# Performance work log

Hardware: AMD Instinct MI355X
Metric: run time of the kernel (lower is better)

Reference implementation:

```python
import jax, jax.numpy as jnp
import numpy as np
import math

DIM = 2048
N_HEADS = 32
N_KV_HEADS = 8
HEAD_DIM = DIM // N_HEADS  # 64
N_REP = N_HEADS // N_KV_HEADS  # 4
BATCH = 1
SEQ = 2048


def rope_cos_sin(seq_len, head_dim, dtype=jnp.float32):
    inv_freq = 1.0 / (10000.0 ** (jnp.arange(0, head_dim, 2, dtype=jnp.float32) / head_dim))
    t = jnp.arange(seq_len, dtype=jnp.float32)
    freqs = jnp.outer(t, inv_freq)            # [S, D/2]
    emb = jnp.concatenate([freqs, freqs], -1)  # [S, D]
    return jnp.cos(emb).astype(dtype), jnp.sin(emb).astype(dtype)


def rotate_half(x):
    x1 = x[..., ::2]
    x2 = x[..., 1::2]
    return jnp.concatenate([-x2, x1], axis=-1)


def setup_inputs() -> dict:
    key = jax.random.key(0)
    ks = jax.random.split(key, 5)
    scale = 1.0 / math.sqrt(DIM)
    x = jax.random.normal(ks[0], (BATCH, SEQ, DIM), jnp.float32)
    wq = jax.random.normal(ks[1], (DIM, N_HEADS * HEAD_DIM), jnp.float32) * scale
    wk = jax.random.normal(ks[2], (DIM, N_KV_HEADS * HEAD_DIM), jnp.float32) * scale
    wv = jax.random.normal(ks[3], (DIM, N_KV_HEADS * HEAD_DIM), jnp.float32) * scale
    wo = jax.random.normal(ks[4], (N_HEADS * HEAD_DIM, DIM), jnp.float32) * scale
    mask = jnp.tril(jnp.ones((SEQ, SEQ), jnp.int32))[None, None]  # [1,1,S,S]
    return {"x": x, "mask": mask, "wq": wq, "wk": wk, "wv": wv, "wo": wo}


def reference(x, mask, wq, wk, wv, wo):
    B, S, _ = x.shape
    q = (x @ wq).reshape(B, S, N_HEADS, HEAD_DIM).transpose(0, 2, 1, 3)     # [B,H,S,D]
    k = (x @ wk).reshape(B, S, N_KV_HEADS, HEAD_DIM).transpose(0, 2, 1, 3)  # [B,Hkv,S,D]
    v = (x @ wv).reshape(B, S, N_KV_HEADS, HEAD_DIM).transpose(0, 2, 1, 3)
    cos, sin = rope_cos_sin(S, HEAD_DIM)  # [S,D]
    q = q * cos + rotate_half(q) * sin
    k = k * cos + rotate_half(k) * sin
    if N_REP > 1:
        k = jnp.repeat(k, N_REP, axis=1)
        v = jnp.repeat(v, N_REP, axis=1)
    scores = jnp.einsum("bhqd,bhkd->bhqk", q, k) / math.sqrt(HEAD_DIM)
    scores = jnp.where(mask == 0, -jnp.inf, scores)
    attn = jax.nn.softmax(scores, axis=-1)
    out = jnp.einsum("bhqk,bhkd->bhqd", attn, v)  # [B,H,S,D]
    out = out.transpose(0, 2, 1, 3).reshape(B, S, N_HEADS * HEAD_DIM)
    return out @ wo
```

## Files before the change

### kernel.cpp

```cpp
#include <hip/hip_runtime.h>
#include <hip/hip_bf16.h>

#define DIM 2048
#define SEQ 2048
#define NH 32
#define HD 64
#define NKV 8
#define QKV_LD 3072

typedef __attribute__((ext_vector_type(8))) short bf16x8;
typedef __attribute__((ext_vector_type(4))) float f32x4;
typedef unsigned short ushort_t;

__device__ inline unsigned short f2bf(float f) {
    union { float f; unsigned int u; } v; v.f = f;
    unsigned int r = v.u + 0x7fffu + ((v.u >> 16) & 1u);
    return (unsigned short)(r >> 16);
}
__device__ inline float bf2f(ushort_t u) {
    union { unsigned int u; float f; } v; v.u = ((unsigned int)u) << 16; return v.f;
}

__device__ inline void async_cp16(const void* g, void* l) {
    __builtin_amdgcn_global_load_lds(
        (const __attribute__((address_space(1))) unsigned int*)g,
        (__attribute__((address_space(3))) unsigned int*)l, 16, 0, 0);
}
__device__ inline void lgkm_fence() {
    __asm__ volatile("s_waitcnt lgkmcnt(0)" ::: "memory");
}

__global__ __launch_bounds__(256) void convert_kernel(
    const float* __restrict__ X, ushort_t* __restrict__ Xb)
{
    int i = (blockIdx.x * 256 + threadIdx.x) * 4;
    float4 v = *(const float4*)(X + i);
    ushort_t o[4] = { f2bf(v.x), f2bf(v.y), f2bf(v.z), f2bf(v.w) };
    *(uint2*)(Xb + i) = *(uint2*)o;
}

__global__ __launch_bounds__(256) void transpose_kernel(
    const float* __restrict__ W, ushort_t* __restrict__ WT, int N)
{
    __shared__ __align__(16) ushort_t tile[64][72];
    const int n0 = blockIdx.x * 64, k0 = blockIdx.y * 64;
    const int t = threadIdx.x;
    {
        const int tk = t >> 4;
        const int tn = (t & 15) * 4;
        #pragma unroll
        for (int i = 0; i < 4; i++) {
            const int k = tk + i * 16;
            float4 v = *(const float4*)(W + (size_t)(k0 + k) * N + n0 + tn);
            tile[tn + 0][k] = f2bf(v.x);
            tile[tn + 1][k] = f2bf(v.y);
            tile[tn + 2][k] = f2bf(v.z);
            tile[tn + 3][k] = f2bf(v.w);
        }
    }
    __syncthreads();
    {
        const int tn = t >> 2;
        const int tk = (t & 3) * 16;
        uint4 a = *(const uint4*)&tile[tn][tk];
        uint4 b = *(const uint4*)&tile[tn][tk + 8];
        ushort_t* dst = WT + (size_t)(n0 + tn) * DIM + k0 + tk;
        *(uint4*)dst = a;
        *(uint4*)(dst + 8) = b;
    }
}

template<int OUT_F32>
__global__ __launch_bounds__(256) void gemm_kernel(
    const ushort_t* __restrict__ A, const ushort_t* __restrict__ BT,
    void* __restrict__ Cout, int K, int lda, int ldo)
{
    __shared__ __align__(16) ushort_t sA[128 * 32];
    __shared__ __align__(16) ushort_t sB[128 * 32];
    const int tn = blockIdx.x * 128, tm = blockIdx.y * 128;
    const int t = threadIdx.x, wave = t >> 6, lane = t & 63;
    const int m16 = lane & 15, quad = lane >> 4;
    const int wr = (wave >> 1) * 64, wc = (wave & 1) * 64;
    const int srow = lane >> 2;
    const int sce = (lane & 3) * 8;

    f32x4 acc[4][4] = {};

    for (int k0 = 0; k0 < K; k0 += 32) {
        __syncthreads();
        #pragma unroll
        for (int p = 0; p < 2; p++) {
            const int j = wave * 2 + p;
            const int row = j * 16 + srow;
            async_cp16(A  + (size_t)(tm + row) * lda + k0 + sce, &sA[j * 512]);
            async_cp16(BT + (size_t)(tn + row) * K   + k0 + sce, &sB[j * 512]);
        }
        __syncthreads();
        bf16x8 af[4], bf[4];
        #pragma unroll
        for (int mt = 0; mt < 4; mt++)
            af[mt] = *(const bf16x8*)&sA[(wr + mt * 16 + m16) * 32 + quad * 8];
        #pragma unroll
        for (int nt = 0; nt < 4; nt++)
            bf[nt] = *(const bf16x8*)&sB[(wc + nt * 16 + m16) * 32 + quad * 8];
        #pragma unroll
        for (int mt = 0; mt < 4; mt++)
            #pragma unroll
            for (int nt = 0; nt < 4; nt++)
                acc[mt][nt] = __builtin_amdgcn_mfma_f32_16x16x32_bf16(af[mt], bf[nt], acc[mt][nt], 0, 0, 0);
    }

    #pragma unroll
    for (int mt = 0; mt < 4; mt++) {
        const int row = tm + wr + mt * 16 + quad * 4;
        #pragma unroll
        for (int nt = 0; nt < 4; nt++) {
            const int col = tn + wc + nt * 16 + m16;
            #pragma unroll
            for (int r = 0; r < 4; r++) {
                if (OUT_F32)
                    ((float*)Cout)[(size_t)(row + r) * ldo + col] = acc[mt][nt][r];
                else
                    ((ushort_t*)Cout)[(size_t)(row + r) * ldo + col] = f2bf(acc[mt][nt][r]);
            }
        }
    }
}

__global__ __launch_bounds__(256) void rope_kernel(ushort_t* qkv, ushort_t* __restrict__ Kr)
{
    const int gid = blockIdx.x * 256 + threadIdx.x;
    const int lane = gid & 63;
    const int idx = gid >> 6;
    const int s = idx / 40;
    const int hh = idx - s * 40;

    const ushort_t* src;
    ushort_t* dst;
    if (hh < 32) {
        dst = qkv + (size_t)s * QKV_LD + hh * 64;
        src = dst;
    } else {
        src = qkv + (size_t)s * QKV_LD + 2048 + (hh - 32) * 64;
        dst = Kr + ((size_t)(hh - 32) * SEQ + s) * 64;
    }

    const float e = bf2f(src[lane]);
    const int i = lane & 31;
    const float freq = __expf(-(float)i * 0.28782313662425572f);
    const float ang = (float)s * freq;
    const float cv = cosf(ang), sv = sinf(ang);
    const int partner = (lane < 32) ? (2 * lane + 1) : (2 * (lane - 32));
    const float y = __shfl(e, partner, 64);
    const float out = (lane < 32) ? (e * cv - y * sv) : (e * cv + y * sv);
    dst[lane] = f2bf(out);
}

__global__ __launch_bounds__(256) void vtrans_kernel(
    const ushort_t* __restrict__ qkv, ushort_t* __restrict__ Vt)
{
    __shared__ __align__(16) ushort_t tile[64][72];
    const int kvh = blockIdx.x & 7;
    const int s0 = (blockIdx.x >> 3) * 64;
    const int t = threadIdx.x;
    {
        const int sr = t >> 3;
        const int d8 = (t & 7) * 8;
        #pragma unroll
        for (int i = 0; i < 2; i++) {
            const int s = sr + i * 32;
            ushort_t tmp[8];
            *(uint4*)tmp = *(const uint4*)(qkv + (size_t)(s0 + s) * QKV_LD + 2560 + kvh * 64 + d8);
            #pragma unroll
            for (int j = 0; j < 8; j++) tile[d8 + j][s] = tmp[j];
        }
    }
    __syncthreads();
    {
        const int dr = t >> 3;
        const int s8 = (t & 7) * 8;
        #pragma unroll
        for (int i = 0; i < 2; i++) {
            const int d = dr + i * 32;
            *(uint4*)(Vt + ((size_t)kvh * 64 + d) * SEQ + s0 + s8) = *(const uint4*)&tile[d][s8];
        }
    }
}

#define SPS 80
__global__ __launch_bounds__(128) void attn_kernel(
    ushort_t* qkv, const ushort_t* __restrict__ Kr, const ushort_t* __restrict__ Vt)
{
    __shared__ __align__(16) ushort_t sP[2][2][16 * SPS];

    const int t = threadIdx.x, wave = t >> 6, lane = t & 63;
    const int m16 = lane & 15, quad = lane >> 4;
    const int h = blockIdx.x & 31;
    const int pair = blockIdx.x >> 5;
    const int kvh = h >> 2;

    const ushort_t* Krh = Kr + (size_t)kvh * SEQ * 64;
    const ushort_t* Vth = Vt + (size_t)kvh * 64 * SEQ;

    #pragma unroll
    for (int ph = 0; ph < 2; ph++) {
        const int qt = ph ? (31 - pair) : pair;
        const int qb = qt * 64;
        const int nkt = qt + 1;

        bf16x8 qf[2][2];
        #pragma unroll
        for (int qa = 0; qa < 2; qa++) {
            const int q0 = qb + (wave + qa * 2) * 16;
            const ushort_t* qp = qkv + (size_t)(q0 + m16) * QKV_LD + h * 64 + quad * 8;
            qf[qa][0] = *(const bf16x8*)qp;
            qf[qa][1] = *(const bf16x8*)(qp + 32);
        }

        f32x4 oacc[2][4] = {};
        float m_run[2] = { -1e30f, -1e30f };
        float l_run[2] = { 0.f, 0.f };

        for (int kt = 0; kt < nkt; kt++) {
            const int kbase = kt * 64;
            const bool domask = (kt == nkt - 1);

            bf16x8 kf[4][2], vf[4][2];
            #pragma unroll
            for (int knt = 0; knt < 4; knt++) {
                const ushort_t* kp = Krh + (size_t)(kbase + knt * 16 + m16) * 64 + quad * 8;
                kf[knt][0] = *(const bf16x8*)kp;
                kf[knt][1] = *(const bf16x8*)(kp + 32);
            }
            #pragma unroll
            for (int nt = 0; nt < 4; nt++) {
                const ushort_t* vp = Vth + (size_t)(nt * 16 + m16) * SEQ + kbase + quad * 8;
                vf[nt][0] = *(const bf16x8*)vp;
                vf[nt][1] = *(const bf16x8*)(vp + 32);
            }

            #pragma unroll
            for (int qa = 0; qa < 2; qa++) {
                const int qi = qb + (wave + qa * 2) * 16 + m16;

                f32x4 sc[4] = {};
                #pragma unroll
                for (int knt = 0; knt < 4; knt++) {
                    sc[knt] = __builtin_amdgcn_mfma_f32_16x16x32_bf16(kf[knt][0], qf[qa][0], sc[knt], 0, 0, 0);
                    sc[knt] = __builtin_amdgcn_mfma_f32_16x16x32_bf16(kf[knt][1], qf[qa][1], sc[knt], 0, 0, 0);
                }

                float s[16];
                #pragma unroll
                for (int knt = 0; knt < 4; knt++)
                    #pragma unroll
                    for (int r = 0; r < 4; r++) {
                        float v = sc[knt][r] * 0.125f;
                        if (domask && (kbase + knt * 16 + quad * 4 + r > qi)) v = -1e30f;
                        s[knt * 4 + r] = v;
                    }

                float rmax = s[0];
                #pragma unroll
                for (int i = 1; i < 16; i++) rmax = fmaxf(rmax, s[i]);
                rmax = fmaxf(rmax, __shfl_xor(rmax, 16, 64));
                rmax = fmaxf(rmax, __shfl_xor(rmax, 32, 64));

                const float mnew = fmaxf(m_run[qa], rmax);
                const float alpha = __expf(m_run[qa] - mnew);
                m_run[qa] = mnew;

                float ps = 0.f;
                #pragma unroll
                for (int i = 0; i < 16; i++) { s[i] = __expf(s[i] - mnew); ps += s[i]; }
                ps += __shfl_xor(ps, 16, 64);
                ps += __shfl_xor(ps, 32, 64);
                l_run[qa] = l_run[qa] * alpha + ps;

                ushort_t* sPw = sP[wave][(kt * 2 + qa) & 1];
                #pragma unroll
                for (int knt = 0; knt < 4; knt++) {
                    unsigned int u0 = (unsigned int)f2bf(s[knt * 4 + 0]) | ((unsigned int)f2bf(s[knt * 4 + 1]) << 16);
                    unsigned int u1 = (unsigned int)f2bf(s[knt * 4 + 2]) | ((unsigned int)f2bf(s[knt * 4 + 3]) << 16);
                    uint2 pk; pk.x = u0; pk.y = u1;
                    *(uint2*)&sPw[m16 * SPS + knt * 16 + quad * 4] = pk;
                }
                lgkm_fence();
                bf16x8 pf0 = *(const bf16x8*)&sPw[m16 * SPS + quad * 8];
                bf16x8 pf1 = *(const bf16x8*)&sPw[m16 * SPS + 32 + quad * 8];

                #pragma unroll
                for (int nt = 0; nt < 4; nt++) {
                    #pragma unroll
                    for (int r = 0; r < 4; r++) oacc[qa][nt][r] *= alpha;
                    oacc[qa][nt] = __builtin_amdgcn_mfma_f32_16x16x32_bf16(vf[nt][0], pf0, oacc[qa][nt], 0, 0, 0);
                    oacc[qa][nt] = __builtin_amdgcn_mfma_f32_16x16x32_bf16(vf[nt][1], pf1, oacc[qa][nt], 0, 0, 0);
                }
            }
        }

        #pragma unroll
        for (int qa = 0; qa < 2; qa++) {
            const int q = qb + (wave + qa * 2) * 16 + m16;
            const float rl = 1.f / l_run[qa];
            #pragma unroll
            for (int nt = 0; nt < 4; nt++) {
                ushort_t pk[4];
                #pragma unroll
                for (int r = 0; r < 4; r++) pk[r] = f2bf(oacc[qa][nt][r] * rl);
                *(uint2*)&qkv[(size_t)q * QKV_LD + h * 64 + nt * 16 + quad * 4] = *(uint2*)pk;
            }
        }
    }
}

extern "C" void kernel_launch(void* const* d_in, const int* in_sizes, int n_in,
                              void* d_out, int out_size, void* d_ws, size_t ws_size,
                              hipStream_t stream)
{
    const float* x  = (const float*)d_in[0];
    const float* wq = (const float*)d_in[2];
    const float* wk = (const float*)d_in[3];
    const float* wv = (const float*)d_in[4];
    const float* wo = (const float*)d_in[5];

    ushort_t* WT  = (ushort_t*)d_ws;
    ushort_t* xb  = WT + (size_t)3072 * 2048;
    ushort_t* woT = xb;
    ushort_t* qkv = xb + (size_t)2048 * 2048;
    ushort_t* Kr  = qkv + (size_t)SEQ * QKV_LD;
    ushort_t* Vt  = Kr + (size_t)NKV * SEQ * HD;

    dim3 blk(256);

    convert_kernel<<<(DIM * SEQ) / 1024, blk, 0, stream>>>(x, xb);
    transpose_kernel<<<dim3(32, 32), blk, 0, stream>>>(wq, WT, 2048);
    transpose_kernel<<<dim3(8, 32),  blk, 0, stream>>>(wk, WT + (size_t)2048 * 2048, 512);
    transpose_kernel<<<dim3(8, 32),  blk, 0, stream>>>(wv, WT + (size_t)2560 * 2048, 512);

    gemm_kernel<0><<<dim3(QKV_LD / 128, SEQ / 128), blk, 0, stream>>>(xb, WT, qkv, DIM, DIM, QKV_LD);

    transpose_kernel<<<dim3(32, 32), blk, 0, stream>>>(wo, woT, 2048);

    rope_kernel<<<(SEQ * 40 * 64) / 256, blk, 0, stream>>>(qkv, Kr);
    vtrans_kernel<<<NKV * (SEQ / 64), blk, 0, stream>>>(qkv, Vt);

    attn_kernel<<<16 * NH, dim3(128), 0, stream>>>(qkv, Kr, Vt);

    gemm_kernel<1><<<dim3(DIM / 128, SEQ / 128), blk, 0, stream>>>(qkv, woT, d_out, DIM, QKV_LD, DIM);
}
```

Baseline: 312.1 us.

## Restructure attention to one q-tile per 4-wave block, heaviest tiles first

Changes the attention work split: each block now handles a single 64-row query tile with four waves of 16 rows each, instead of two waves processing a paired light/heavy tile with two 16-row sub-tiles each. Blocks are ordered so the longest causal tiles launch first, and the grid doubles to 1024 blocks of 256 threads. V loads are moved after the QK MFMAs to overlap them with compute. This raises parallelism and lowers per-wave register use, but each K/V fragment is now reused by only one query sub-tile per wave, which increases global load traffic.

```diff
diff --git a/kernel.cpp b/kernel.cpp
--- a/kernel.cpp
+++ b/kernel.cpp
@@ -188,128 +188,119 @@
 }
 
 #define SPS 80
-__global__ __launch_bounds__(128) void attn_kernel(
+__global__ __launch_bounds__(256, 4) void attn_kernel(
     ushort_t* qkv, const ushort_t* __restrict__ Kr, const ushort_t* __restrict__ Vt)
 {
-    __shared__ __align__(16) ushort_t sP[2][2][16 * SPS];
+    __shared__ __align__(16) ushort_t sP[4][2][16 * SPS];
 
     const int t = threadIdx.x, wave = t >> 6, lane = t & 63;
     const int m16 = lane & 15, quad = lane >> 4;
     const int h = blockIdx.x & 31;
-    const int pair = blockIdx.x >> 5;
+    const int qt = 31 - (blockIdx.x >> 5);
     const int kvh = h >> 2;
 
     const ushort_t* Krh = Kr + (size_t)kvh * SEQ * 64;
     const ushort_t* Vth = Vt + (size_t)kvh * 64 * SEQ;
 
-    #pragma unroll
-    for (int ph = 0; ph < 2; ph++) {
-        const int qt = ph ? (31 - pair) : pair;
-        const int qb = qt * 64;
-        const int nkt = qt + 1;
-
-        bf16x8 qf[2][2];
-        #pragma unroll
-        for (int qa = 0; qa < 2; qa++) {
-            const int q0 = qb + (wave + qa * 2) * 16;
-            const ushort_t* qp = qkv + (size_t)(q0 + m16) * QKV_LD + h * 64 + quad * 8;
-            qf[qa][0] = *(const bf16x8*)qp;
-            qf[qa][1] = *(const bf16x8*)(qp + 32);
-        }
-
-        f32x4 oacc[2][4] = {};
-        float m_run[2] = { -1e30f, -1e30f };
-        float l_run[2] = { 0.f, 0.f };
-
-        for (int kt = 0; kt < nkt; kt++) {
-            const int kbase = kt * 64;
-            const bool domask = (kt == nkt - 1);
-
-            bf16x8 kf[4][2], vf[4][2];
-            #pragma unroll
-            for (int knt = 0; knt < 4; knt++) {
-                const ushort_t* kp = Krh + (size_t)(kbase + knt * 16 + m16) * 64 + quad * 8;
-                kf[knt][0] = *(const bf16x8*)kp;
-                kf[knt][1] = *(const bf16x8*)(kp + 32);
+    const int qb = qt * 64;
+    const int q0 = qb + wave * 16;
+    const int qi = q0 + m16;
+    const int nkt = qt + 1;
+
+    bf16x8 qf[2];
+    {
+        const ushort_t* qp = qkv + (size_t)qi * QKV_LD + h * 64 + quad * 8;
+        qf[0] = *(const bf16x8*)qp;
+        qf[1] = *(const bf16x8*)(qp + 32);
+    }
+
+    f32x4 oacc[4] = {};
+    float m_run = -1e30f;
+    float l_run = 0.f;
+
+    for (int kt = 0; kt < nkt; kt++) {
+        const int kbase = kt * 64;
+        const bool domask = (kt == nkt - 1);
+
+        bf16x8 kf[4][2];
+        #pragma unroll
+        for (int knt = 0; knt < 4; knt++) {
+            const ushort_t* kp = Krh + (size_t)(kbase + knt * 16 + m16) * 64 + quad * 8;
+            kf[knt][0] = *(const bf16x8*)kp;
+            kf[knt][1] = *(const bf16x8*)(kp + 32);
+        }
+
+        f32x4 sc[4] = {};
+        #pragma unroll
+        for (int knt = 0; knt < 4; knt++) {
+            sc[knt] = __builtin_amdgcn_mfma_f32_16x16x32_bf16(kf[knt][0], qf[0], sc[knt], 0, 0, 0);
+            sc[knt] = __builtin_amdgcn_mfma_f32_16x16x32_bf16(kf[knt][1], qf[1], sc[knt], 0, 0, 0);
+        }
+
+        bf16x8 vf[4][2];
+        #pragma unroll
+        for (int nt = 0; nt < 4; nt++) {
+            const ushort_t* vp = Vth + (size_t)(nt * 16 + m16) * SEQ + kbase + quad * 8;
+            vf[nt][0] = *(const bf16x8*)vp;
+            vf[nt][1] = *(const bf16x8*)(vp + 32);
+        }
+
+        float s[16];
+        #pragma unroll
+        for (int knt = 0; knt < 4; knt++)
+            #pragma unroll
+            for (int r = 0; r < 4; r++) {
+                float v = sc[knt][r] * 0.125f;
+                if (domask && (kbase + knt * 16 + quad * 4 + r > qi)) v = -1e30f;
+                s[knt * 4 + r] = v;
             }
-            #pragma unroll
-            for (int nt = 0; nt < 4; nt++) {
-                const ushort_t* vp = Vth + (size_t)(nt * 16 + m16) * SEQ + kbase + quad * 8;
-                vf[nt][0] = *(const bf16x8*)vp;
-                vf[nt][1] = *(const bf16x8*)(vp + 32);
-            }
-
-            #pragma unroll
-            for (int qa = 0; qa < 2; qa++) {
-                const int qi = qb + (wave + qa * 2) * 16 + m16;
-
-                f32x4 sc[4] = {};
-                #pragma unroll
-                for (int knt = 0; knt < 4; knt++) {
-                    sc[knt] = __builtin_amdgcn_mfma_f32_16x16x32_bf16(kf[knt][0], qf[qa][0], sc[knt], 0, 0, 0);
-                    sc[knt] = __builtin_amdgcn_mfma_f32_16x16x32_bf16(kf[knt][1], qf[qa][1], sc[knt], 0, 0, 0);
-                }
-
-                float s[16];
-                #pragma unroll
-                for (int knt = 0; knt < 4; knt++)
-                    #pragma unroll
-                    for (int r = 0; r < 4; r++) {
-                        float v = sc[knt][r] * 0.125f;
-                        if (domask && (kbase + knt * 16 + quad * 4 + r > qi)) v = -1e30f;
-                        s[knt * 4 + r] = v;
-                    }
-
-                float rmax = s[0];
-                #pragma unroll
-                for (int i = 1; i < 16; i++) rmax = fmaxf(rmax, s[i]);
-                rmax = fmaxf(rmax, __shfl_xor(rmax, 16, 64));
-                rmax = fmaxf(rmax, __shfl_xor(rmax, 32, 64));
-
-                const float mnew = fmaxf(m_run[qa], rmax);
-                const float alpha = __expf(m_run[qa] - mnew);
-                m_run[qa] = mnew;
-
-                float ps = 0.f;
-                #pragma unroll
-                for (int i = 0; i < 16; i++) { s[i] = __expf(s[i] - mnew); ps += s[i]; }
-                ps += __shfl_xor(ps, 16, 64);
-                ps += __shfl_xor(ps, 32, 64);
-                l_run[qa] = l_run[qa] * alpha + ps;
-
-                ushort_t* sPw = sP[wave][(kt * 2 + qa) & 1];
-                #pragma unroll
-                for (int knt = 0; knt < 4; knt++) {
-                    unsigned int u0 = (unsigned int)f2bf(s[knt * 4 + 0]) | ((unsigned int)f2bf(s[knt * 4 + 1]) << 16);
-                    unsigned int u1 = (unsigned int)f2bf(s[knt * 4 + 2]) | ((unsigned int)f2bf(s[knt * 4 + 3]) << 16);
-                    uint2 pk; pk.x = u0; pk.y = u1;
-                    *(uint2*)&sPw[m16 * SPS + knt * 16 + quad * 4] = pk;
-                }
-                lgkm_fence();
-                bf16x8 pf0 = *(const bf16x8*)&sPw[m16 * SPS + quad * 8];
-                bf16x8 pf1 = *(const bf16x8*)&sPw[m16 * SPS + 32 + quad * 8];
-
-                #pragma unroll
-                for (int nt = 0; nt < 4; nt++) {
-                    #pragma unroll
-                    for (int r = 0; r < 4; r++) oacc[qa][nt][r] *= alpha;
-                    oacc[qa][nt] = __builtin_amdgcn_mfma_f32_16x16x32_bf16(vf[nt][0], pf0, oacc[qa][nt], 0, 0, 0);
-                    oacc[qa][nt] = __builtin_amdgcn_mfma_f32_16x16x32_bf16(vf[nt][1], pf1, oacc[qa][nt], 0, 0, 0);
-                }
-            }
-        }
-
-        #pragma unroll
-        for (int qa = 0; qa < 2; qa++) {
-            const int q = qb + (wave + qa * 2) * 16 + m16;
-            const float rl = 1.f / l_run[qa];
-            #pragma unroll
-            for (int nt = 0; nt < 4; nt++) {
-                ushort_t pk[4];
-                #pragma unroll
-                for (int r = 0; r < 4; r++) pk[r] = f2bf(oacc[qa][nt][r] * rl);
-                *(uint2*)&qkv[(size_t)q * QKV_LD + h * 64 + nt * 16 + quad * 4] = *(uint2*)pk;
-            }
+
+        float rmax = s[0];
+        #pragma unroll
+        for (int i = 1; i < 16; i++) rmax = fmaxf(rmax, s[i]);
+        rmax = fmaxf(rmax, __shfl_xor(rmax, 16, 64));
+        rmax = fmaxf(rmax, __shfl_xor(rmax, 32, 64));
+
+        const float mnew = fmaxf(m_run, rmax);
+        const float alpha = __expf(m_run - mnew);
+        m_run = mnew;
+
+        float ps = 0.f;
+        #pragma unroll
+        for (int i = 0; i < 16; i++) { s[i] = __expf(s[i] - mnew); ps += s[i]; }
+        ps += __shfl_xor(ps, 16, 64);
+        ps += __shfl_xor(ps, 32, 64);
+        l_run = l_run * alpha + ps;
+
+        ushort_t* sPw = sP[wave][kt & 1];
+        #pragma unroll
+        for (int knt = 0; knt < 4; knt++) {
+            unsigned int u0 = (unsigned int)f2bf(s[knt * 4 + 0]) | ((unsigned int)f2bf(s[knt * 4 + 1]) << 16);
+            unsigned int u1 = (unsigned int)f2bf(s[knt * 4 + 2]) | ((unsigned int)f2bf(s[knt * 4 + 3]) << 16);
+            uint2 pk; pk.x = u0; pk.y = u1;
+            *(uint2*)&sPw[m16 * SPS + knt * 16 + quad * 4] = pk;
+        }
+        lgkm_fence();
+        bf16x8 pf0 = *(const bf16x8*)&sPw[m16 * SPS + quad * 8];
+        bf16x8 pf1 = *(const bf16x8*)&sPw[m16 * SPS + 32 + quad * 8];
+
+        #pragma unroll
+        for (int nt = 0; nt < 4; nt++) {
+            #pragma unroll
+            for (int r = 0; r < 4; r++) oacc[nt][r] *= alpha;
+            oacc[nt] = __builtin_amdgcn_mfma_f32_16x16x32_bf16(vf[nt][0], pf0, oacc[nt], 0, 0, 0);
+            oacc[nt] = __builtin_amdgcn_mfma_f32_16x16x32_bf16(vf[nt][1], pf1, oacc[nt], 0, 0, 0);
+        }
+    }
+
+    {
+        const float rl = 1.f / l_run;
+        #pragma unroll
+        for (int nt = 0; nt < 4; nt++) {
+            ushort_t pk[4];
+            #pragma unroll
+            for (int r = 0; r < 4; r++) pk[r] = f2bf(oacc[nt][r] * rl);
+            *(uint2*)&qkv[(size_t)qi * QKV_LD + h * 64 + nt * 16 + quad * 4] = *(uint2*)pk;
         }
     }
 }
@@ -345,7 +336,7 @@
     rope_kernel<<<(SEQ * 40 * 64) / 256, blk, 0, stream>>>(qkv, Kr);
     vtrans_kernel<<<NKV * (SEQ / 64), blk, 0, stream>>>(qkv, Vt);
 
-    attn_kernel<<<16 * NH, dim3(128), 0, stream>>>(qkv, Kr, Vt);
+    attn_kernel<<<32 * NH, dim3(256), 0, stream>>>(qkv, Kr, Vt);
 
     gemm_kernel<1><<<dim3(DIM / 128, SEQ / 128), blk, 0, stream>>>(qkv, woT, d_out, DIM, QKV_LD, DIM);
 }
```

Result: slower. 377.7 us (+21.0%).

## Restructure attention into 512-thread blocks with 128-row bands and K prefetch

Applied to the files above, without the earlier changes.

The attention kernel moves from 128-thread blocks that each process two 64-row query tiles in sequence to 512-thread blocks. Each block runs two wave groups at once, one on band p and one on band 15-p, so work stays balanced under the causal mask. Each wave covers 32 query rows in a 128-row band, and the next K tile is loaded into registers while the current scores are computed. The block skips the fully masked last key tile for the first query sub-row and uses tree reductions for the row max and sum. In exchange the grid shrinks to 256 blocks and register pressure rises under launch_bounds(512,2).

```diff
diff --git a/kernel.cpp b/kernel.cpp
--- a/kernel.cpp
+++ b/kernel.cpp
@@ -188,128 +188,148 @@
 }
 
 #define SPS 80
-__global__ __launch_bounds__(128) void attn_kernel(
+__global__ __launch_bounds__(512, 2) void attn_kernel(
     ushort_t* qkv, const ushort_t* __restrict__ Kr, const ushort_t* __restrict__ Vt)
 {
-    __shared__ __align__(16) ushort_t sP[2][2][16 * SPS];
+    __shared__ __align__(16) ushort_t sP[8][2][16 * SPS];
 
     const int t = threadIdx.x, wave = t >> 6, lane = t & 63;
     const int m16 = lane & 15, quad = lane >> 4;
     const int h = blockIdx.x & 31;
-    const int pair = blockIdx.x >> 5;
+    const int p = blockIdx.x >> 5;
+    const int grp = wave >> 2;
+    const int w4 = wave & 3;
+    const int band = grp ? p : 15 - p;
     const int kvh = h >> 2;
 
     const ushort_t* Krh = Kr + (size_t)kvh * SEQ * 64;
     const ushort_t* Vth = Vt + (size_t)kvh * 64 * SEQ;
 
+    const int nkt = band * 2 + 2;
+
+    int qi[2];
+    bf16x8 qf[2][2];
     #pragma unroll
-    for (int ph = 0; ph < 2; ph++) {
-        const int qt = ph ? (31 - pair) : pair;
-        const int qb = qt * 64;
-        const int nkt = qt + 1;
-
-        bf16x8 qf[2][2];
+    for (int qa = 0; qa < 2; qa++) {
+        qi[qa] = band * 128 + (w4 + qa * 4) * 16 + m16;
+        const ushort_t* qp = qkv + (size_t)qi[qa] * QKV_LD + h * 64 + quad * 8;
+        qf[qa][0] = *(const bf16x8*)qp;
+        qf[qa][1] = *(const bf16x8*)(qp + 32);
+    }
+
+    f32x4 oacc[2][4] = {};
+    float m_run[2] = { -1e30f, -1e30f };
+    float l_run[2] = { 0.f, 0.f };
+
+    bf16x8 kf[4][2];
+    #pragma unroll
+    for (int knt = 0; knt < 4; knt++) {
+        const ushort_t* kp = Krh + (size_t)(knt * 16 + m16) * 64 + quad * 8;
+        kf[knt][0] = *(const bf16x8*)kp;
+        kf[knt][1] = *(const bf16x8*)(kp + 32);
+    }
+
+    for (int kt = 0; kt < nkt; kt++) {
+        const int kbase = kt * 64;
+        const bool last = (kt == nkt - 1);
+
+        f32x4 sc[2][4] = {};
         #pragma unroll
         for (int qa = 0; qa < 2; qa++) {
-            const int q0 = qb + (wave + qa * 2) * 16;
-            const ushort_t* qp = qkv + (size_t)(q0 + m16) * QKV_LD + h * 64 + quad * 8;
-            qf[qa][0] = *(const bf16x8*)qp;
-            qf[qa][1] = *(const bf16x8*)(qp + 32);
-        }
-
-        f32x4 oacc[2][4] = {};
-        float m_run[2] = { -1e30f, -1e30f };
-        float l_run[2] = { 0.f, 0.f };
-
-        for (int kt = 0; kt < nkt; kt++) {
-            const int kbase = kt * 64;
-            const bool domask = (kt == nkt - 1);
-
-            bf16x8 kf[4][2], vf[4][2];
+            if (qa == 0 && last) continue;
             #pragma unroll
             for (int knt = 0; knt < 4; knt++) {
-                const ushort_t* kp = Krh + (size_t)(kbase + knt * 16 + m16) * 64 + quad * 8;
+                sc[qa][knt] = __builtin_amdgcn_mfma_f32_16x16x32_bf16(kf[knt][0], qf[qa][0], sc[qa][knt], 0, 0, 0);
+                sc[qa][knt] = __builtin_amdgcn_mfma_f32_16x16x32_bf16(kf[knt][1], qf[qa][1], sc[qa][knt], 0, 0, 0);
+            }
+        }
+
+        bf16x8 vf[4][2];
+        #pragma unroll
+        for (int nt = 0; nt < 4; nt++) {
+            const ushort_t* vp = Vth + (size_t)(nt * 16 + m16) * SEQ + kbase + quad * 8;
+            vf[nt][0] = *(const bf16x8*)vp;
+            vf[nt][1] = *(const bf16x8*)(vp + 32);
+        }
+        if (!last) {
+            #pragma unroll
+            for (int knt = 0; knt < 4; knt++) {
+                const ushort_t* kp = Krh + (size_t)(kbase + 64 + knt * 16 + m16) * 64 + quad * 8;
                 kf[knt][0] = *(const bf16x8*)kp;
                 kf[knt][1] = *(const bf16x8*)(kp + 32);
             }
+        }
+
+        #pragma unroll
+        for (int qa = 0; qa < 2; qa++) {
+            if (qa == 0 && last) continue;
+            const bool domask = (qa == 0) ? (kt == nkt - 2) : last;
+
+            float s[16];
+            #pragma unroll
+            for (int knt = 0; knt < 4; knt++)
+                #pragma unroll
+                for (int r = 0; r < 4; r++) {
+                    float v = sc[qa][knt][r] * 0.125f;
+                    if (domask && (kbase + knt * 16 + quad * 4 + r > qi[qa])) v = -1e30f;
+                    s[knt * 4 + r] = v;
+                }
+
+            float x0 = fmaxf(s[0], s[1]),  x1 = fmaxf(s[2], s[3]);
+            float x2 = fmaxf(s[4], s[5]),  x3 = fmaxf(s[6], s[7]);
+            float x4 = fmaxf(s[8], s[9]),  x5 = fmaxf(s[10], s[11]);
+            float x6 = fmaxf(s[12], s[13]), x7 = fmaxf(s[14], s[15]);
+            float rmax = fmaxf(fmaxf(fmaxf(x0, x1), fmaxf(x2, x3)),
+                               fmaxf(fmaxf(x4, x5), fmaxf(x6, x7)));
+            rmax = fmaxf(rmax, __shfl_xor(rmax, 16, 64));
+            rmax = fmaxf(rmax, __shfl_xor(rmax, 32, 64));
+
+            const float mnew = fmaxf(m_run[qa], rmax);
+            const float alpha = __expf(m_run[qa] - mnew);
+            m_run[qa] = mnew;
+
+            #pragma unroll
+            for (int i = 0; i < 16; i++) s[i] = __expf(s[i] - mnew);
+            float y0 = s[0] + s[1],  y1 = s[2] + s[3];
+            float y2 = s[4] + s[5],  y3 = s[6] + s[7];
+            float y4 = s[8] + s[9],  y5 = s[10] + s[11];
+            float y6 = s[12] + s[13], y7 = s[14] + s[15];
+            float ps = ((y0 + y1) + (y2 + y3)) + ((y4 + y5) + (y6 + y7));
+            ps += __shfl_xor(ps, 16, 64);
+            ps += __shfl_xor(ps, 32, 64);
+            l_run[qa] = l_run[qa] * alpha + ps;
+
+            ushort_t* sPw = sP[wave][qa];
+            #pragma unroll
+            for (int knt = 0; knt < 4; knt++) {
+                unsigned int u0 = (unsigned int)f2bf(s[knt * 4 + 0]) | ((unsigned int)f2bf(s[knt * 4 + 1]) << 16);
+                unsigned int u1 = (unsigned int)f2bf(s[knt * 4 + 2]) | ((unsigned int)f2bf(s[knt * 4 + 3]) << 16);
+                uint2 pk; pk.x = u0; pk.y = u1;
+                *(uint2*)&sPw[m16 * SPS + knt * 16 + quad * 4] = pk;
+            }
+            lgkm_fence();
+            bf16x8 pf0 = *(const bf16x8*)&sPw[m16 * SPS + quad * 8];
+            bf16x8 pf1 = *(const bf16x8*)&sPw[m16 * SPS + 32 + quad * 8];
+
             #pragma unroll
             for (int nt = 0; nt < 4; nt++) {
-                const ushort_t* vp = Vth + (size_t)(nt * 16 + m16) * SEQ + kbase + quad * 8;
-                vf[nt][0] = *(const bf16x8*)vp;
-                vf[nt][1] = *(const bf16x8*)(vp + 32);
-            }
-
-            #pragma unroll
-            for (int qa = 0; qa < 2; qa++) {
-                const int qi = qb + (wave + qa * 2) * 16 + m16;
-
-                f32x4 sc[4] = {};
                 #pragma unroll
-                for (int knt = 0; knt < 4; knt++) {
-                    sc[knt] = __builtin_amdgcn_mfma_f32_16x16x32_bf16(kf[knt][0], qf[qa][0], sc[knt], 0, 0, 0);
-                    sc[knt] = __builtin_amdgcn_mfma_f32_16x16x32_bf16(kf[knt][1], qf[qa][1], sc[knt], 0, 0, 0);
-                }
-
-                float s[16];
-                #pragma unroll
-                for (int knt = 0; knt < 4; knt++)
-                    #pragma unroll
-                    for (int r = 0; r < 4; r++) {
-                        float v = sc[knt][r] * 0.125f;
-                        if (domask && (kbase + knt * 16 + quad * 4 + r > qi)) v = -1e30f;
-                        s[knt * 4 + r] = v;
-                    }
-
-                float rmax = s[0];
-                #pragma unroll
-                for (int i = 1; i < 16; i++) rmax = fmaxf(rmax, s[i]);
-                rmax = fmaxf(rmax, __shfl_xor(rmax, 16, 64));
-                rmax = fmaxf(rmax, __shfl_xor(rmax, 32, 64));
-
-                const float mnew = fmaxf(m_run[qa], rmax);
-                const float alpha = __expf(m_run[qa] - mnew);
-                m_run[qa] = mnew;
-
-                float ps = 0.f;
-                #pragma unroll
-                for (int i = 0; i < 16; i++) { s[i] = __expf(s[i] - mnew); ps += s[i]; }
-                ps += __shfl_xor(ps, 16, 64);
-                ps += __shfl_xor(ps, 32, 64);
-                l_run[qa] = l_run[qa] * alpha + ps;
-
-                ushort_t* sPw = sP[wave][(kt * 2 + qa) & 1];
-                #pragma unroll
-                for (int knt = 0; knt < 4; knt++) {
-                    unsigned int u0 = (unsigned int)f2bf(s[knt * 4 + 0]) | ((unsigned int)f2bf(s[knt * 4 + 1]) << 16);
-                    unsigned int u1 = (unsigned int)f2bf(s[knt * 4 + 2]) | ((unsigned int)f2bf(s[knt * 4 + 3]) << 16);
-                    uint2 pk; pk.x = u0; pk.y = u1;
-                    *(uint2*)&sPw[m16 * SPS + knt * 16 + quad * 4] = pk;
-                }
-                lgkm_fence();
-                bf16x8 pf0 = *(const bf16x8*)&sPw[m16 * SPS + quad * 8];
-                bf16x8 pf1 = *(const bf16x8*)&sPw[m16 * SPS + 32 + quad * 8];
-
-                #pragma unroll
-                for (int nt = 0; nt < 4; nt++) {
-                    #pragma unroll
-                    for (int r = 0; r < 4; r++) oacc[qa][nt][r] *= alpha;
-                    oacc[qa][nt] = __builtin_amdgcn_mfma_f32_16x16x32_bf16(vf[nt][0], pf0, oacc[qa][nt], 0, 0, 0);
-                    oacc[qa][nt] = __builtin_amdgcn_mfma_f32_16x16x32_bf16(vf[nt][1], pf1, oacc[qa][nt], 0, 0, 0);
-                }
-            }
-        }
-
-        #pragma unroll
-        for (int qa = 0; qa < 2; qa++) {
-            const int q = qb + (wave + qa * 2) * 16 + m16;
-            const float rl = 1.f / l_run[qa];
-            #pragma unroll
-            for (int nt = 0; nt < 4; nt++) {
-                ushort_t pk[4];
-                #pragma unroll
-                for (int r = 0; r < 4; r++) pk[r] = f2bf(oacc[qa][nt][r] * rl);
-                *(uint2*)&qkv[(size_t)q * QKV_LD + h * 64 + nt * 16 + quad * 4] = *(uint2*)pk;
-            }
+                for (int r = 0; r < 4; r++) oacc[qa][nt][r] *= alpha;
+                oacc[qa][nt] = __builtin_amdgcn_mfma_f32_16x16x32_bf16(vf[nt][0], pf0, oacc[qa][nt], 0, 0, 0);
+                oacc[qa][nt] = __builtin_amdgcn_mfma_f32_16x16x32_bf16(vf[nt][1], pf1, oacc[qa][nt], 0, 0, 0);
+            }
+        }
+    }
+
+    #pragma unroll
+    for (int qa = 0; qa < 2; qa++) {
+        const float rl = 1.f / l_run[qa];
+        #pragma unroll
+        for (int nt = 0; nt < 4; nt++) {
+            ushort_t pk[4];
+            #pragma unroll
+            for (int r = 0; r < 4; r++) pk[r] = f2bf(oacc[qa][nt][r] * rl);
+            *(uint2*)&qkv[(size_t)qi[qa] * QKV_LD + h * 64 + nt * 16 + quad * 4] = *(uint2*)pk;
         }
     }
 }
@@ -345,7 +365,7 @@
     rope_kernel<<<(SEQ * 40 * 64) / 256, blk, 0, stream>>>(qkv, Kr);
     vtrans_kernel<<<NKV * (SEQ / 64), blk, 0, stream>>>(qkv, Vt);
 
-    attn_kernel<<<16 * NH, dim3(128), 0, stream>>>(qkv, Kr, Vt);
+    attn_kernel<<<8 * NH, dim3(512), 0, stream>>>(qkv, Kr, Vt);
 
     gemm_kernel<1><<<dim3(DIM / 128, SEQ / 128), blk, 0, stream>>>(qkv, woT, d_out, DIM, QKV_LD, DIM);
 }
```

Result: faster. 301.5 us (-3.4%).
